# Kernel tuning notes

Hardware: AMD Instinct MI355X
Metric: run time of the kernel (lower is better)

The kernel has to match this reference:

```python
import jax, jax.numpy as jnp
import numpy as np

LN_EPS = 1e-5

def _moe_forward(x, Wg, bg, W1, b1, W2, b2, ln_w, ln_b, gate_scale, top_k=2):
    B, N, D = x.shape
    E = Wg.shape[1]
    x_flat = x.reshape(B * N, D)                      # [T, D]
    # --- router (MoEGate): softmax -> top-k -> renormalize ---
    logits = x_flat @ Wg + bg                         # [T, E]
    probs = jax.nn.softmax(logits, axis=-1)
    w, idx = jax.lax.top_k(probs, top_k)              # [T, k]
    w = w / jnp.sum(w, axis=-1, keepdims=True)
    # dense gate matrix [T, E]: scatter top-k weights onto their experts
    gates = jnp.sum(jax.nn.one_hot(idx, E, dtype=x.dtype) * w[..., None], axis=1)
    # --- experts: Linear -> GELU(erf) -> Linear, computed densely for all experts ---
    h = jax.nn.gelu(jnp.einsum('td,edo->eto', x_flat, W1) + b1[:, None, :],
                    approximate=False)                # [E, T, O]
    eo = jnp.einsum('eto,eoq->etq', h, W2) + b2[:, None, :]  # [E, T, O]
    # --- weighted combine (equivalent to masked scatter-add in the torch loop) ---
    out_flat = jnp.einsum('te,eto->to', gates, eo)    # [T, O]
    out = out_flat.reshape(B, N, -1) * gate_scale[0]
    # --- LayerNorm ---
    mu = jnp.mean(out, axis=-1, keepdims=True)
    var = jnp.var(out, axis=-1, keepdims=True)
    return (out - mu) / jnp.sqrt(var + LN_EPS) * ln_w + ln_b


def setup_inputs() -> dict:
    key = jax.random.key(0)
    ks = jax.random.split(key, 5)
    B, N, D, O, E = 8, 1024, 1024, 4096, 4
    return {
        'x': jax.random.normal(ks[0], (B, N, D), dtype=jnp.float32),
        'Wg': jax.random.normal(ks[1], (D, E), dtype=jnp.float32) * 0.02,
        'bg': jnp.zeros((E,), jnp.float32),
        'W1': jax.random.normal(ks[2], (E, D, O), dtype=jnp.float32) * (1.0 / np.sqrt(D)),
        'b1': jnp.zeros((E, O), jnp.float32),
        'W2': jax.random.normal(ks[3], (E, O, O), dtype=jnp.float32) * (1.0 / np.sqrt(O)),
        'b2': jnp.zeros((E, O), jnp.float32),
        'ln_w': jnp.ones((O,), jnp.float32),
        'ln_b': jnp.zeros((O,), jnp.float32),
        'gate_scale': jnp.ones((1,), jnp.float32) * 0.1,
    }


def reference(x, Wg, bg, W1, b1, W2, b2, ln_w, ln_b, gate_scale):
    return _moe_forward(x, Wg, bg, W1, b1, W2, b2, ln_w, ln_b, gate_scale)
```

## Files before the change

kernel.cpp:

```cpp
#include <hip/hip_runtime.h>
#include <cmath>


typedef float f32x4 __attribute__((ext_vector_type(4)));
typedef __bf16 bf16x8 __attribute__((ext_vector_type(8)));
typedef __bf16 bf16x4 __attribute__((ext_vector_type(4)));

#define T_TOK 8192
#define DDIM 1024
#define ODIM 4096
#define NEXP 4

__device__ __forceinline__ void gl_lds16(const void* g, void* l) {
    __builtin_amdgcn_global_load_lds(
        (const __attribute__((address_space(1))) void*)g,
        (__attribute__((address_space(3))) void*)l, 16, 0, 0);
}

__global__ __launch_bounds__(256) void cvt_bf16_vec(const float* __restrict__ in,
                                                    __bf16* __restrict__ out, int n4) {
    int i = blockIdx.x * 256 + threadIdx.x;
    if (i >= n4) return;
    float4 v = ((const float4*)in)[i];
    bf16x4 o = { (__bf16)v.x, (__bf16)v.y, (__bf16)v.z, (__bf16)v.w };
    ((bf16x4*)out)[i] = o;
}

__global__ __launch_bounds__(256) void transpose_cvt(const float* __restrict__ in,
                                                     __bf16* __restrict__ out,
                                                     int R, int C) {
    __shared__ float tile[32][33];
    const size_t eoff = (size_t)blockIdx.z * R * C;
    const float* ip = in + eoff;
    __bf16* op = out + eoff;
    const int c0 = blockIdx.x * 32, r0 = blockIdx.y * 32;
    const int tx = threadIdx.x, ty = threadIdx.y;
#pragma unroll
    for (int i = 0; i < 4; i++)
        tile[ty + i * 8][tx] = ip[(size_t)(r0 + ty + i * 8) * C + c0 + tx];
    __syncthreads();
#pragma unroll
    for (int i = 0; i < 4; i++)
        op[(size_t)(c0 + ty + i * 8) * R + r0 + tx] = (__bf16)tile[tx][ty + i * 8];
}

__global__ __launch_bounds__(256) void router_kernel(const float* __restrict__ x,
                                                     const float* __restrict__ Wg,
                                                     const float* __restrict__ bg,
                                                     int* __restrict__ counts,
                                                     int* __restrict__ perm,
                                                     float* __restrict__ wlist) {
    const int wave = threadIdx.x >> 6, lane = threadIdx.x & 63;
    const int t = blockIdx.x * 4 + wave;
    const float* xr = x + (size_t)t * DDIM;
    float a0 = 0.f, a1 = 0.f, a2 = 0.f, a3 = 0.f;
    const float4* Wg4 = (const float4*)Wg;
    for (int d = lane; d < DDIM; d += 64) {
        float xv = xr[d];
        float4 w = Wg4[d];
        a0 += xv * w.x; a1 += xv * w.y; a2 += xv * w.z; a3 += xv * w.w;
    }
#pragma unroll
    for (int off = 32; off; off >>= 1) {
        a0 += __shfl_xor(a0, off); a1 += __shfl_xor(a1, off);
        a2 += __shfl_xor(a2, off); a3 += __shfl_xor(a3, off);
    }
    if (lane == 0) {
        float l[4] = {a0 + bg[0], a1 + bg[1], a2 + bg[2], a3 + bg[3]};
        float mx = fmaxf(fmaxf(l[0], l[1]), fmaxf(l[2], l[3]));
        float p[4], s = 0.f;
#pragma unroll
        for (int e = 0; e < 4; e++) { p[e] = expf(l[e] - mx); s += p[e]; }
#pragma unroll
        for (int e = 0; e < 4; e++) p[e] /= s;
        int e1 = 0;
#pragma unroll
        for (int e = 1; e < 4; e++) if (p[e] > p[e1]) e1 = e;
        int e2 = (e1 == 0) ? 1 : 0;
#pragma unroll
        for (int e = 0; e < 4; e++) if (e != e1 && p[e] > p[e2]) e2 = e;
        const float inv = 1.0f / (p[e1] + p[e2]);
        int pos1 = atomicAdd(&counts[e1], 1);
        perm[e1 * T_TOK + pos1] = t;
        wlist[e1 * T_TOK + pos1] = p[e1] * inv;
        int pos2 = atomicAdd(&counts[e2], 1);
        perm[e2 * T_TOK + pos2] = t;
        wlist[e2 * T_TOK + pos2] = p[e2] * inv;
    }
}


#define STAGE_A(t, h, bb)                                                      \
  if ((t) < NT) {                                                              \
    gl_lds16(pa##h##0 + (size_t)(t) * BK, &As[bb][h][w * 512]);                \
    gl_lds16(pa##h##1 + (size_t)(t) * BK, &As[bb][h][w * 512 + 4096]);         \
  }
#define STAGE_B(t, h, bb)                                                      \
  if ((t) < NT) {                                                              \
    gl_lds16(pb##h##0 + (size_t)(t) * BK, &Bs[bb][h][w * 512]);                \
    gl_lds16(pb##h##1 + (size_t)(t) * BK, &Bs[bb][h][w * 512 + 4096]);         \
  }
#define LDA(bb, mg, kk) (*(const bf16x8*)&As[bb][wr][(mg)*1024 + rowOff + offK##kk])
#define LDB(bb, nn, kk) (*(const bf16x8*)&Bs[bb][wch][(nn)*1024 + rowBOff + offK##kk])
#define MFMA4(p, nn)                                                           \
  acc[2*(p)][nn]   = __builtin_amdgcn_mfma_f32_16x16x32_bf16(af0k0, bfr[nn][0], acc[2*(p)][nn], 0, 0, 0);   \
  acc[2*(p)][nn]   = __builtin_amdgcn_mfma_f32_16x16x32_bf16(af0k1, bfr[nn][1], acc[2*(p)][nn], 0, 0, 0);   \
  acc[2*(p)+1][nn] = __builtin_amdgcn_mfma_f32_16x16x32_bf16(af1k0, bfr[nn][0], acc[2*(p)+1][nn], 0, 0, 0); \
  acc[2*(p)+1][nn] = __builtin_amdgcn_mfma_f32_16x16x32_bf16(af1k1, bfr[nn][1], acc[2*(p)+1][nn], 0, 0, 0);
#define PHASE_TAIL(p)                                                          \
  __builtin_amdgcn_s_barrier();                                                \
  asm volatile("s_waitcnt lgkmcnt(0)" ::: "memory");                           \
  __builtin_amdgcn_s_setprio(1);                                               \
  MFMA4(p, 0) MFMA4(p, 1) MFMA4(p, 2) MFMA4(p, 3)                              \
  __builtin_amdgcn_s_setprio(0);                                               \
  __builtin_amdgcn_s_barrier();
#define TILE(bb, t)                                                            \
  {                                                                            \
    bfr[0][0] = LDB(bb, 0, 0); bfr[0][1] = LDB(bb, 0, 1);                      \
    bfr[1][0] = LDB(bb, 1, 0); bfr[1][1] = LDB(bb, 1, 1);                      \
    bfr[2][0] = LDB(bb, 2, 0); bfr[2][1] = LDB(bb, 2, 1);                      \
    bfr[3][0] = LDB(bb, 3, 0); bfr[3][1] = LDB(bb, 3, 1);                      \
    af0k0 = LDA(bb, 0, 0); af0k1 = LDA(bb, 0, 1);                              \
    af1k0 = LDA(bb, 1, 0); af1k1 = LDA(bb, 1, 1);                              \
    STAGE_A((t) + 1, 0, (bb) ^ 1)                                              \
    PHASE_TAIL(0)                                                              \
    af0k0 = LDA(bb, 2, 0); af0k1 = LDA(bb, 2, 1);                              \
    af1k0 = LDA(bb, 3, 0); af1k1 = LDA(bb, 3, 1);                              \
    STAGE_A((t) + 1, 1, (bb) ^ 1)                                              \
    PHASE_TAIL(1)                                                              \
    af0k0 = LDA(bb, 4, 0); af0k1 = LDA(bb, 4, 1);                              \
    af1k0 = LDA(bb, 5, 0); af1k1 = LDA(bb, 5, 1);                              \
    STAGE_B((t) + 2, 0, bb)                                                    \
    PHASE_TAIL(2)                                                              \
    af0k0 = LDA(bb, 6, 0); af0k1 = LDA(bb, 6, 1);                              \
    af1k0 = LDA(bb, 7, 0); af1k1 = LDA(bb, 7, 1);                              \
    STAGE_B((t) + 2, 1, bb)                                                    \
    if ((t) + 2 < NT) { asm volatile("s_waitcnt vmcnt(4)" ::: "memory"); }     \
    else              { asm volatile("s_waitcnt vmcnt(0)" ::: "memory"); }     \
    PHASE_TAIL(3)                                                              \
  }

template <int MODE, int KDIM>
__global__ __launch_bounds__(512, 2) void moe_gemm256(
    const __bf16* __restrict__ A, const __bf16* __restrict__ B,
    const float* __restrict__ bias, __bf16* __restrict__ Hout,
    float* __restrict__ Fout, const int* __restrict__ perm,
    const float* __restrict__ wlist, const int* __restrict__ countp) {
    constexpr int BK = 64;
    constexpr int NT = KDIM / BK;
    constexpr int GX = ODIM / 256;

    __shared__ __align__(16) __bf16 As[2][2][128 * 64];
    __shared__ __align__(16) __bf16 Bs[2][2][128 * 64];

    const int count = *countp;
    const int nAy = (count + 255) >> 8;
    const int na = nAy * GX;
    int lin = blockIdx.y * GX + blockIdx.x;
    if (lin >= na) return;
    {
        const int q = na >> 3, r = na & 7;
        const int xcd = lin & 7, loc = lin >> 3;
        lin = xcd * q + (xcd < r ? xcd : r) + loc;
    }
    const int bx = lin & (GX - 1), by = lin / GX;
    const int m0 = by * 256, n0 = bx * 256;

    const int tid = threadIdx.x;
    const int w = tid >> 6, lane = tid & 63;
    const int r16 = lane & 15, quad = lane >> 4;
    const int wr = w >> 2;
    const int wc = w & 3;
    const int wch = wc >> 1;

    const int swz = r16 & 7;
    const int offK0 = ((quad) ^ swz) * 8;
    const int offK1 = ((quad + 4) ^ swz) * 8;
    const int rowOff = r16 * 64;
    const int rowBOff = (wc & 1) * 4096 + rowOff;

    const int srow = tid >> 3;
    const int sq = ((tid & 7) ^ (srow & 7)) * 8;
    const __bf16 *pa00, *pa01, *pa10, *pa11;
    if (MODE == 0) {
        pa00 = A + (size_t)perm[m0 + srow] * KDIM + sq;
        pa01 = A + (size_t)perm[m0 + 64 + srow] * KDIM + sq;
        pa10 = A + (size_t)perm[m0 + 128 + srow] * KDIM + sq;
        pa11 = A + (size_t)perm[m0 + 192 + srow] * KDIM + sq;
    } else {
        pa00 = A + (size_t)(m0 + srow) * KDIM + sq;
        pa01 = A + (size_t)(m0 + 64 + srow) * KDIM + sq;
        pa10 = A + (size_t)(m0 + 128 + srow) * KDIM + sq;
        pa11 = A + (size_t)(m0 + 192 + srow) * KDIM + sq;
    }
    const __bf16* pb00 = B + (size_t)(n0 + srow) * KDIM + sq;
    const __bf16* pb01 = B + (size_t)(n0 + 64 + srow) * KDIM + sq;
    const __bf16* pb10 = B + (size_t)(n0 + 128 + srow) * KDIM + sq;
    const __bf16* pb11 = B + (size_t)(n0 + 192 + srow) * KDIM + sq;

    f32x4 acc[8][4] = {};
    bf16x8 bfr[4][2];
    bf16x8 af0k0, af0k1, af1k0, af1k1;

    STAGE_B(0, 0, 0) STAGE_B(0, 1, 0)
    STAGE_A(0, 0, 0) STAGE_A(0, 1, 0)
    STAGE_B(1, 0, 1) STAGE_B(1, 1, 1)
    asm volatile("s_waitcnt vmcnt(4)" ::: "memory");
    __builtin_amdgcn_s_barrier();

    for (int t = 0; t < NT; t += 2) {
        TILE(0, t)
        TILE(1, t + 1)
    }

    const int colBase = n0 + wc * 64 + r16;
    const int rowW = m0 + wr * 128 + quad * 4;
    if (MODE == 0) {
#pragma unroll
        for (int mg = 0; mg < 8; mg++) {
            const int rowBase = rowW + mg * 16;
#pragma unroll
            for (int n = 0; n < 4; n++) {
                const int col = colBase + n * 16;
                const float bv = bias[col];
#pragma unroll
                for (int r = 0; r < 4; r++) {
                    if (rowBase + r < count) {
                        float xv = acc[mg][n][r] + bv;
                        float u = 1.5957691216057308f * xv * (1.0f + 0.044715f * xv * xv);
                        float gv = xv * __builtin_amdgcn_rcpf(1.0f + __expf(-u));
                        Hout[(size_t)(rowBase + r) * ODIM + col] = (__bf16)gv;
                    }
                }
            }
        }
    } else {
#pragma unroll
        for (int mg = 0; mg < 8; mg++) {
            const int rowBase = rowW + mg * 16;
            int tok[4]; float g[4]; bool ok[4];
#pragma unroll
            for (int r = 0; r < 4; r++) {
                const int i = rowBase + r;
                ok[r] = (i < count);
                tok[r] = ok[r] ? perm[i] : 0;
                g[r] = ok[r] ? wlist[i] : 0.f;
            }
#pragma unroll
            for (int n = 0; n < 4; n++) {
                const int col = colBase + n * 16;
                const float bv = bias[col];
#pragma unroll
                for (int r = 0; r < 4; r++) {
                    if (ok[r]) {
                        float v = g[r] * (acc[mg][n][r] + bv);
                        Fout[(size_t)tok[r] * ODIM + col] += v;
                    }
                }
            }
        }
    }
}

#undef STAGE_A
#undef STAGE_B
#undef LDA
#undef LDB
#undef MFMA4
#undef PHASE_TAIL
#undef TILE

__global__ __launch_bounds__(256) void ln_kernel(float* __restrict__ out,
                                                 const float* __restrict__ lw,
                                                 const float* __restrict__ lb,
                                                 const float* __restrict__ gsp) {
    const int t = blockIdx.x;
    float* row = out + (size_t)t * ODIM;
    const float gs = gsp[0];
    float4 v[4];
    float s = 0.f, ss = 0.f;
#pragma unroll
    for (int i = 0; i < 4; i++) {
        float4 a = ((const float4*)row)[threadIdx.x + i * 256];
        a.x *= gs; a.y *= gs; a.z *= gs; a.w *= gs;
        v[i] = a;
        s += a.x + a.y + a.z + a.w;
        ss += a.x * a.x + a.y * a.y + a.z * a.z + a.w * a.w;
    }
#pragma unroll
    for (int off = 32; off; off >>= 1) {
        s += __shfl_xor(s, off);
        ss += __shfl_xor(ss, off);
    }
    __shared__ float rs[4], rss[4];
    const int wave = threadIdx.x >> 6, lane = threadIdx.x & 63;
    if (lane == 0) { rs[wave] = s; rss[wave] = ss; }
    __syncthreads();
    s = rs[0] + rs[1] + rs[2] + rs[3];
    ss = rss[0] + rss[1] + rss[2] + rss[3];
    const float mu = s * (1.0f / ODIM);
    const float var = ss * (1.0f / ODIM) - mu * mu;
    const float inv = 1.0f / sqrtf(var + 1e-5f);
#pragma unroll
    for (int i = 0; i < 4; i++) {
        const int c4 = threadIdx.x + i * 256;
        float4 w4 = ((const float4*)lw)[c4];
        float4 b4 = ((const float4*)lb)[c4];
        float4 o;
        o.x = (v[i].x - mu) * inv * w4.x + b4.x;
        o.y = (v[i].y - mu) * inv * w4.y + b4.y;
        o.z = (v[i].z - mu) * inv * w4.z + b4.z;
        o.w = (v[i].w - mu) * inv * w4.w + b4.w;
        ((float4*)row)[c4] = o;
    }
}

extern "C" void kernel_launch(void* const* d_in, const int* in_sizes, int n_in,
                              void* d_out, int out_size, void* d_ws, size_t ws_size,
                              hipStream_t stream) {
    const float* x   = (const float*)d_in[0];
    const float* Wg  = (const float*)d_in[1];
    const float* bg  = (const float*)d_in[2];
    const float* W1  = (const float*)d_in[3];
    const float* b1  = (const float*)d_in[4];
    const float* W2  = (const float*)d_in[5];
    const float* b2  = (const float*)d_in[6];
    const float* lnw = (const float*)d_in[7];
    const float* lnb = (const float*)d_in[8];
    const float* gsc = (const float*)d_in[9];
    float* out = (float*)d_out;

    char* w = (char*)d_ws;
    __bf16* Xb  = (__bf16*)w;
    __bf16* W1T = Xb + (size_t)T_TOK * DDIM;
    __bf16* W2T = W1T + (size_t)NEXP * ODIM * DDIM;
    __bf16* H   = W2T + (size_t)NEXP * ODIM * ODIM;
    int*   counts = (int*)(H + (size_t)T_TOK * ODIM);
    int*   perm   = counts + NEXP;
    float* wlist  = (float*)(perm + NEXP * T_TOK);

    hipMemsetAsync(counts, 0, (NEXP + 2 * NEXP * T_TOK) * sizeof(int) , stream);
    hipMemsetAsync(out, 0, (size_t)T_TOK * ODIM * sizeof(float), stream);

    cvt_bf16_vec<<<(T_TOK * DDIM / 4) / 256, 256, 0, stream>>>(x, Xb, T_TOK * DDIM / 4);
    dim3 tb(32, 8);
    transpose_cvt<<<dim3(ODIM / 32, DDIM / 32, NEXP), tb, 0, stream>>>(W1, W1T, DDIM, ODIM);
    transpose_cvt<<<dim3(ODIM / 32, ODIM / 32, NEXP), tb, 0, stream>>>(W2, W2T, ODIM, ODIM);
    router_kernel<<<T_TOK / 4, 256, 0, stream>>>(x, Wg, bg, counts, perm, wlist);

    for (int e = 0; e < NEXP; e++) {
        moe_gemm256<0, DDIM><<<dim3(ODIM / 256, T_TOK / 256), 512, 0, stream>>>(
            Xb, W1T + (size_t)e * ODIM * DDIM, b1 + e * ODIM,
            H, nullptr, perm + e * T_TOK, nullptr, counts + e);
        moe_gemm256<1, ODIM><<<dim3(ODIM / 256, T_TOK / 256), 512, 0, stream>>>(
            H, W2T + (size_t)e * ODIM * ODIM, b2 + e * ODIM,
            nullptr, out, perm + e * T_TOK, wlist + e * T_TOK, counts + e);
    }
    ln_kernel<<<T_TOK, 256, 0, stream>>>(out, lnw, lnb, gsc);
}
```

Before: 2.234 ms.

## Merge per-expert GEMM launches into single grouped launches with atomic combine

Result: faster. 1.910 ms (-14.5%).

```diff
diff --git a/kernel.cpp b/kernel.cpp
--- a/kernel.cpp
+++ b/kernel.cpp
@@ -114,6 +114,15 @@
   MFMA4(p, 0) MFMA4(p, 1) MFMA4(p, 2) MFMA4(p, 3)                              \
   __builtin_amdgcn_s_setprio(0);                                               \
   __builtin_amdgcn_s_barrier();
+#define PHASE_TAIL3(p, t)                                                      \
+  __builtin_amdgcn_s_barrier();                                                \
+  asm volatile("s_waitcnt lgkmcnt(0)" ::: "memory");                           \
+  __builtin_amdgcn_s_setprio(1);                                               \
+  MFMA4(p, 0) MFMA4(p, 1) MFMA4(p, 2) MFMA4(p, 3)                              \
+  __builtin_amdgcn_s_setprio(0);                                               \
+  if ((t) + 2 < NT) { asm volatile("s_waitcnt vmcnt(4)" ::: "memory"); }       \
+  else              { asm volatile("s_waitcnt vmcnt(0)" ::: "memory"); }       \
+  __builtin_amdgcn_s_barrier();
 #define TILE(bb, t)                                                            \
   {                                                                            \
     bfr[0][0] = LDB(bb, 0, 0); bfr[0][1] = LDB(bb, 0, 1);                      \
@@ -135,36 +144,50 @@
     af0k0 = LDA(bb, 6, 0); af0k1 = LDA(bb, 6, 1);                              \
     af1k0 = LDA(bb, 7, 0); af1k1 = LDA(bb, 7, 1);                              \
     STAGE_B((t) + 2, 1, bb)                                                    \
-    if ((t) + 2 < NT) { asm volatile("s_waitcnt vmcnt(4)" ::: "memory"); }     \
-    else              { asm volatile("s_waitcnt vmcnt(0)" ::: "memory"); }     \
-    PHASE_TAIL(3)                                                              \
+    PHASE_TAIL3(3, t)                                                          \
   }
 
 template <int MODE, int KDIM>
 __global__ __launch_bounds__(512, 2) void moe_gemm256(
-    const __bf16* __restrict__ A, const __bf16* __restrict__ B,
-    const float* __restrict__ bias, __bf16* __restrict__ Hout,
-    float* __restrict__ Fout, const int* __restrict__ perm,
-    const float* __restrict__ wlist, const int* __restrict__ countp) {
+    const __bf16* __restrict__ A, const __bf16* __restrict__ Ball,
+    const float* __restrict__ biasAll, __bf16* __restrict__ Hout,
+    float* __restrict__ Fout, const int* __restrict__ permAll,
+    const float* __restrict__ wlistAll, const int* __restrict__ countsAll,
+    int e0, int nE, int HROWS) {
     constexpr int BK = 64;
     constexpr int NT = KDIM / BK;
-    constexpr int GX = ODIM / 256;
 
     __shared__ __align__(16) __bf16 As[2][2][128 * 64];
     __shared__ __align__(16) __bf16 Bs[2][2][128 * 64];
 
-    const int count = *countp;
-    const int nAy = (count + 255) >> 8;
-    const int na = nAy * GX;
-    int lin = blockIdx.y * GX + blockIdx.x;
-    if (lin >= na) return;
-    {
-        const int q = na >> 3, r = na & 7;
-        const int xcd = lin & 7, loc = lin >> 3;
-        lin = xcd * q + (xcd < r ? xcd : r) + loc;
-    }
-    const int bx = lin & (GX - 1), by = lin / GX;
-    const int m0 = by * 256, n0 = bx * 256;
+    int cnts[4], cum[5], hs[5];
+    cum[0] = 0; hs[0] = 0;
+#pragma unroll
+    for (int j = 0; j < 4; j++) {
+        int c = (j < nE) ? countsAll[e0 + j] : 0;
+        cnts[j] = c;
+        cum[j + 1] = cum[j] + ((c + 255) >> 8);
+        hs[j + 1] = hs[j] + c;
+    }
+    const int totnb = cum[4];
+    const int na = 16 * totnb;
+    const int b = blockIdx.x;
+    if (b >= na) return;
+    const int xcd = b & 7, loc = b >> 3;
+    const int bx = xcd * 2 + (loc & 1);
+    const int by = loc >> 1;
+    int ei = 0;
+#pragma unroll
+    for (int j = 1; j < 4; j++) if (j < nE && cum[j] <= by) ei = j;
+    const int e = e0 + ei;
+    const int count = cnts[ei];
+    const int m0 = (by - cum[ei]) * 256;
+    const int hstart = hs[ei];
+    const int n0 = bx * 256;
+    const int* __restrict__ perm = permAll + e * T_TOK;
+    const float* __restrict__ wlist = (MODE == 1) ? wlistAll + e * T_TOK : nullptr;
+    const __bf16* __restrict__ B = Ball + (size_t)e * ODIM * KDIM;
+    const float* __restrict__ bias = biasAll + e * ODIM;
 
     const int tid = threadIdx.x;
     const int w = tid >> 6, lane = tid & 63;
@@ -188,10 +211,11 @@
         pa10 = A + (size_t)perm[m0 + 128 + srow] * KDIM + sq;
         pa11 = A + (size_t)perm[m0 + 192 + srow] * KDIM + sq;
     } else {
-        pa00 = A + (size_t)(m0 + srow) * KDIM + sq;
-        pa01 = A + (size_t)(m0 + 64 + srow) * KDIM + sq;
-        pa10 = A + (size_t)(m0 + 128 + srow) * KDIM + sq;
-        pa11 = A + (size_t)(m0 + 192 + srow) * KDIM + sq;
+        const int rl = HROWS - 1;
+        pa00 = A + (size_t)min(hstart + m0 + srow, rl) * KDIM + sq;
+        pa01 = A + (size_t)min(hstart + m0 + 64 + srow, rl) * KDIM + sq;
+        pa10 = A + (size_t)min(hstart + m0 + 128 + srow, rl) * KDIM + sq;
+        pa11 = A + (size_t)min(hstart + m0 + 192 + srow, rl) * KDIM + sq;
     }
     const __bf16* pb00 = B + (size_t)(n0 + srow) * KDIM + sq;
     const __bf16* pb01 = B + (size_t)(n0 + 64 + srow) * KDIM + sq;
@@ -229,7 +253,7 @@
                         float xv = acc[mg][n][r] + bv;
                         float u = 1.5957691216057308f * xv * (1.0f + 0.044715f * xv * xv);
                         float gv = xv * __builtin_amdgcn_rcpf(1.0f + __expf(-u));
-                        Hout[(size_t)(rowBase + r) * ODIM + col] = (__bf16)gv;
+                        Hout[(size_t)(hstart + rowBase + r) * ODIM + col] = (__bf16)gv;
                     }
                 }
             }
@@ -254,7 +278,7 @@
                 for (int r = 0; r < 4; r++) {
                     if (ok[r]) {
                         float v = g[r] * (acc[mg][n][r] + bv);
-                        Fout[(size_t)tok[r] * ODIM + col] += v;
+                        atomicAdd(&Fout[(size_t)tok[r] * ODIM + col], v);
                     }
                 }
             }
@@ -268,6 +292,7 @@
 #undef LDB
 #undef MFMA4
 #undef PHASE_TAIL
+#undef PHASE_TAIL3
 #undef TILE
 
 __global__ __launch_bounds__(256) void ln_kernel(float* __restrict__ out,
@@ -330,31 +355,63 @@
     const float* gsc = (const float*)d_in[9];
     float* out = (float*)d_out;
 
+    const size_t szH2   = (size_t)2 * T_TOK * ODIM * sizeof(__bf16);
+    const size_t szW2T  = (size_t)NEXP * ODIM * ODIM * sizeof(__bf16);
+    const size_t szXb   = (size_t)T_TOK * DDIM * sizeof(__bf16);
+    const size_t szW1T  = (size_t)NEXP * ODIM * DDIM * sizeof(__bf16);
+    const size_t szH1   = (size_t)T_TOK * ODIM * sizeof(__bf16);
+    const size_t szList = NEXP * sizeof(int) + (size_t)NEXP * T_TOK * 8;
+    const size_t needMerged = szH2 + szW2T + szList;
+
     char* w = (char*)d_ws;
-    __bf16* Xb  = (__bf16*)w;
-    __bf16* W1T = Xb + (size_t)T_TOK * DDIM;
-    __bf16* W2T = W1T + (size_t)NEXP * ODIM * DDIM;
-    __bf16* H   = W2T + (size_t)NEXP * ODIM * ODIM;
-    int*   counts = (int*)(H + (size_t)T_TOK * ODIM);
-    int*   perm   = counts + NEXP;
-    float* wlist  = (float*)(perm + NEXP * T_TOK);
-
-    hipMemsetAsync(counts, 0, (NEXP + 2 * NEXP * T_TOK) * sizeof(int) , stream);
-    hipMemsetAsync(out, 0, (size_t)T_TOK * ODIM * sizeof(float), stream);
-
-    cvt_bf16_vec<<<(T_TOK * DDIM / 4) / 256, 256, 0, stream>>>(x, Xb, T_TOK * DDIM / 4);
-    dim3 tb(32, 8);
-    transpose_cvt<<<dim3(ODIM / 32, DDIM / 32, NEXP), tb, 0, stream>>>(W1, W1T, DDIM, ODIM);
-    transpose_cvt<<<dim3(ODIM / 32, ODIM / 32, NEXP), tb, 0, stream>>>(W2, W2T, ODIM, ODIM);
-    router_kernel<<<T_TOK / 4, 256, 0, stream>>>(x, Wg, bg, counts, perm, wlist);
-
-    for (int e = 0; e < NEXP; e++) {
-        moe_gemm256<0, DDIM><<<dim3(ODIM / 256, T_TOK / 256), 512, 0, stream>>>(
-            Xb, W1T + (size_t)e * ODIM * DDIM, b1 + e * ODIM,
-            H, nullptr, perm + e * T_TOK, nullptr, counts + e);
-        moe_gemm256<1, ODIM><<<dim3(ODIM / 256, T_TOK / 256), 512, 0, stream>>>(
-            H, W2T + (size_t)e * ODIM * ODIM, b2 + e * ODIM,
-            nullptr, out, perm + e * T_TOK, wlist + e * T_TOK, counts + e);
+    const int grid1 = 16 * 67;
+
+    if (ws_size >= needMerged) {
+        __bf16* H   = (__bf16*)w;
+        __bf16* W2T = (__bf16*)(w + szH2);
+        __bf16* Xb  = W2T;
+        __bf16* W1T = (__bf16*)((char*)W2T + szXb);
+        int*   counts = (int*)(w + szH2 + szW2T);
+        int*   perm   = counts + NEXP;
+        float* wlist  = (float*)(perm + NEXP * T_TOK);
+
+        hipMemsetAsync(counts, 0, (NEXP + 2 * NEXP * T_TOK) * sizeof(int), stream);
+        hipMemsetAsync(out, 0, (size_t)T_TOK * ODIM * sizeof(float), stream);
+
+        cvt_bf16_vec<<<(T_TOK * DDIM / 4) / 256, 256, 0, stream>>>(x, Xb, T_TOK * DDIM / 4);
+        dim3 tb(32, 8);
+        transpose_cvt<<<dim3(ODIM / 32, DDIM / 32, NEXP), tb, 0, stream>>>(W1, W1T, DDIM, ODIM);
+        router_kernel<<<T_TOK / 4, 256, 0, stream>>>(x, Wg, bg, counts, perm, wlist);
+
+        moe_gemm256<0, DDIM><<<grid1, 512, 0, stream>>>(
+            Xb, W1T, b1, H, nullptr, perm, nullptr, counts, 0, NEXP, 2 * T_TOK);
+        transpose_cvt<<<dim3(ODIM / 32, ODIM / 32, NEXP), tb, 0, stream>>>(W2, W2T, ODIM, ODIM);
+        moe_gemm256<1, ODIM><<<grid1, 512, 0, stream>>>(
+            H, W2T, b2, nullptr, out, perm, wlist, counts, 0, NEXP, 2 * T_TOK);
+    } else {
+        __bf16* Xb  = (__bf16*)w;
+        __bf16* W1T = (__bf16*)((char*)Xb + szXb);
+        __bf16* W2T = (__bf16*)((char*)W1T + szW1T);
+        __bf16* H   = (__bf16*)((char*)W2T + szW2T);
+        int*   counts = (int*)((char*)H + szH1);
+        int*   perm   = counts + NEXP;
+        float* wlist  = (float*)(perm + NEXP * T_TOK);
+
+        hipMemsetAsync(counts, 0, (NEXP + 2 * NEXP * T_TOK) * sizeof(int), stream);
+        hipMemsetAsync(out, 0, (size_t)T_TOK * ODIM * sizeof(float), stream);
+
+        cvt_bf16_vec<<<(T_TOK * DDIM / 4) / 256, 256, 0, stream>>>(x, Xb, T_TOK * DDIM / 4);
+        dim3 tb(32, 8);
+        transpose_cvt<<<dim3(ODIM / 32, DDIM / 32, NEXP), tb, 0, stream>>>(W1, W1T, DDIM, ODIM);
+        transpose_cvt<<<dim3(ODIM / 32, ODIM / 32, NEXP), tb, 0, stream>>>(W2, W2T, ODIM, ODIM);
+        router_kernel<<<T_TOK / 4, 256, 0, stream>>>(x, Wg, bg, counts, perm, wlist);
+
+        for (int e = 0; e < NEXP; e++) {
+            moe_gemm256<0, DDIM><<<16 * 32, 512, 0, stream>>>(
+                Xb, W1T, b1, H, nullptr, perm, nullptr, counts, e, 1, T_TOK);
+            moe_gemm256<1, ODIM><<<16 * 32, 512, 0, stream>>>(
+                H, W2T, b2, nullptr, out, perm, wlist, counts, e, 1, T_TOK);
+        }
     }
     ln_kernel<<<T_TOK, 256, 0, stream>>>(out, lnw, lnb, gsc);
 }
```
